# Kernel optimization log

Hardware: AMD Instinct MI355X
Metric: run time of the kernel (lower is better)

Reference implementation:

```python
import jax, jax.numpy as jnp
import numpy as np

N_NODES = 50000
N_EDGES = 800000
IN_DIM = 128
HID = 32
HEADS = 4
OUT_DIM = 64
NEG_SLOPE = 0.2
EPS = 1e-16


def _gat_conv(x, src, dst, W, a_src, a_dst, b, heads, ch):
    """PyG GATConv (with self-loops already appended to src/dst), concat=True."""
    N = x.shape[0]
    h = (x @ W).reshape(N, heads, ch)                      # [N,H,C]
    alpha_s = jnp.einsum('nhc,hc->nh', h, a_src)           # [N,H]
    alpha_d = jnp.einsum('nhc,hc->nh', h, a_dst)           # [N,H]
    e = jax.nn.leaky_relu(alpha_s[src] + alpha_d[dst], NEG_SLOPE)  # [E,H]
    emax = jax.ops.segment_max(e, dst, num_segments=N)     # segment softmax over dst
    ex = jnp.exp(e - emax[dst])
    denom = jax.ops.segment_sum(ex, dst, num_segments=N)
    alpha = ex / (denom[dst] + EPS)                        # [E,H]
    out = jax.ops.segment_sum(h[src] * alpha[:, :, None], dst, num_segments=N)
    return out.reshape(N, heads * ch) + b


def setup_inputs() -> dict:
    key = jax.random.key(0)
    ks = jax.random.split(key, 16)
    x = jax.random.normal(ks[0], (N_NODES, IN_DIM), dtype=jnp.float32)
    edge_index = jax.random.randint(ks[1], (2, N_EDGES), 0, N_NODES, dtype=jnp.int64)

    def glorot(k, shape):
        fan = sum(shape[-2:]) if len(shape) > 1 else shape[-1]
        return jax.random.normal(k, shape, dtype=jnp.float32) * np.sqrt(2.0 / fan)

    # layer 0: IN_DIM -> HID x HEADS
    W0 = glorot(ks[2], (IN_DIM, HEADS * HID))
    as0 = glorot(ks[3], (HEADS, HID))
    ad0 = glorot(ks[4], (HEADS, HID))
    b0 = jnp.zeros((HEADS * HID,), jnp.float32)
    # layer 1: HID*HEADS -> HID x HEADS
    W1 = glorot(ks[5], (HEADS * HID, HEADS * HID))
    as1 = glorot(ks[6], (HEADS, HID))
    ad1 = glorot(ks[7], (HEADS, HID))
    b1 = jnp.zeros((HEADS * HID,), jnp.float32)
    # layer 2: HID*HEADS -> OUT_DIM, heads=1
    W2 = glorot(ks[8], (HEADS * HID, OUT_DIM))
    as2 = glorot(ks[9], (1, OUT_DIM))
    ad2 = glorot(ks[10], (1, OUT_DIM))
    b2 = jnp.zeros((OUT_DIM,), jnp.float32)
    return {"x": x, "edge_index": edge_index,
            "W0": W0, "as0": as0, "ad0": ad0, "b0": b0,
            "W1": W1, "as1": as1, "ad1": ad1, "b1": b1,
            "W2": W2, "as2": as2, "ad2": ad2, "b2": b2}


def reference(x, edge_index, W0, as0, ad0, b0, W1, as1, ad1, b1, W2, as2, ad2, b2):
    N = x.shape[0]
    # PyG GATConv default add_self_loops=True
    loops = jnp.arange(N, dtype=edge_index.dtype)
    src = jnp.concatenate([edge_index[0], loops])
    dst = jnp.concatenate([edge_index[1], loops])
    h = _gat_conv(x, src, dst, W0, as0, ad0, b0, HEADS, HID)
    h = _gat_conv(h, src, dst, W1, as1, ad1, b1, HEADS, HID)
    h = _gat_conv(h, src, dst, W2, as2, ad2, b2, 1, OUT_DIM)
    return h
```

## Files before the change

kernel.cpp:

```cpp
#include <hip/hip_runtime.h>
#include <hip/hip_fp16.h>
#include <cstdint>
#include <cstddef>

#define NEG_SLOPE 0.2f
#define EPS_F 1e-16f

static __device__ __forceinline__ float leaky(float x) { return x > 0.f ? x : NEG_SLOPE * x; }


__global__ __launch_bounds__(1024) void scan_k(const int* __restrict__ cnt, int* __restrict__ off, int N) {
    __shared__ int wsum[16];
    int tid = threadIdx.x;
    int lane = tid & 63, wid = tid >> 6;
    int running = 0;
    for (int base = 0; base < N; base += 1024) {
        int i = base + tid;
        int v = (i < N) ? cnt[i] : 0;
        int iv = v;
        #pragma unroll
        for (int d = 1; d < 64; d <<= 1) {
            int t = __shfl_up(iv, d);
            if (lane >= d) iv += t;
        }
        if (lane == 63) wsum[wid] = iv;
        __syncthreads();
        if (tid < 16) {
            int s = wsum[tid];
            #pragma unroll
            for (int d = 1; d < 16; d <<= 1) {
                int t = __shfl_up(s, d);
                if (tid >= d) s += t;
            }
            wsum[tid] = s;
        }
        __syncthreads();
        int add = wid ? wsum[wid - 1] : 0;
        if (i < N) off[i + 1] = running + add + iv;
        int ct = wsum[15];
        __syncthreads();
        running += ct;
    }
    if (tid == 0) off[0] = 0;
}


__global__ __launch_bounds__(256) void partB_k(const int* __restrict__ src, const int* __restrict__ dst,
                                               const int* __restrict__ starts, int* __restrict__ packed,
                                               int E, int nbuk) {
    __shared__ int lcnt[256];
    __shared__ int lbase[256];
    const int blk = blockIdx.x;
    for (int i = threadIdx.x; i < nbuk; i += 256) { lcnt[i] = 0; lbase[i] = starts[i * 256 + blk]; }
    __syncthreads();
    const int chunk = (E + 255) / 256;
    const int base = blk * chunk, end = min(base + chunk, E);
    for (int i = base + (int)threadIdx.x; i < end; i += 256) {
        int d = dst[i], s = src[i];
        int b = d >> 8;
        int slot = atomicAdd(&lcnt[b], 1);
        packed[lbase[b] + slot] = s | ((d & 255) << 16);
    }
}


__global__ __launch_bounds__(256) void partC_k(const int* __restrict__ packed, const int* __restrict__ starts,
                                               int* __restrict__ off, int* __restrict__ esrc,
                                               int N, int E, int nbuk) {
    __shared__ int lcnt[256];
    __shared__ int lpre[256];
    const int b = blockIdx.x;
    const int bstart = starts[b * 256];
    const int bend = (b + 1 < nbuk) ? starts[(b + 1) * 256] : E;
    const int tid = threadIdx.x;
    lcnt[tid] = 0;
    __syncthreads();
    for (int i = bstart + tid; i < bend; i += 256) atomicAdd(&lcnt[packed[i] >> 16], 1);
    __syncthreads();
    if (tid < 64) {
        int v0 = lcnt[tid * 4], v1 = lcnt[tid * 4 + 1], v2 = lcnt[tid * 4 + 2], v3 = lcnt[tid * 4 + 3];
        int s = v0 + v1 + v2 + v3;
        int inc = s;
        #pragma unroll
        for (int d = 1; d < 64; d <<= 1) {
            int t = __shfl_up(inc, d);
            if (tid >= d) inc += t;
        }
        int ex = inc - s;
        lpre[tid * 4] = ex;
        lpre[tid * 4 + 1] = ex + v0;
        lpre[tid * 4 + 2] = ex + v0 + v1;
        lpre[tid * 4 + 3] = ex + v0 + v1 + v2;
    }
    __syncthreads();
    const int n0 = b << 8;
    const int nn = min(256, N - n0);
    if (tid < nn) off[n0 + tid] = bstart + lpre[tid];
    if (b == 0 && tid == 0) off[N] = E;
    lcnt[tid] = 0;
    __syncthreads();
    for (int i = bstart + tid; i < bend; i += 256) {
        int p = packed[i];
        int ld = p >> 16;
        int slot = atomicAdd(&lcnt[ld], 1);
        esrc[bstart + lpre[ld] + slot] = p & 0xFFFF;
    }
}


template <int M, int H>
__device__ __forceinline__ void gemm_body(float* xsT, float* wt,
                                          const float* __restrict__ X, const float* __restrict__ W,
                                          const float* __restrict__ a_s, const float* __restrict__ a_d,
                                          __half* __restrict__ O, float* __restrict__ aS,
                                          float* __restrict__ aD, int N, int bid) {
    constexpr int K = 128, BK = 16, ROWS = 128;
    constexpr int CPT = 8;
    constexpr int CT = M / CPT;
    constexpr int RPT = ROWS / (256 / CT);
    constexpr int XP = ROWS + 4;
    constexpr int C = M / H;
    constexpr int REDW = C / CPT;

    const int tid = threadIdx.x;
    const int cc = tid % CT;
    const int rr = tid / CT;
    const int row0 = bid * ROWS;

    float acc[RPT][CPT];
    #pragma unroll
    for (int r = 0; r < RPT; ++r)
        #pragma unroll
        for (int j = 0; j < CPT; ++j) acc[r][j] = 0.f;

    for (int k0 = 0; k0 < K; k0 += BK) {
        #pragma unroll
        for (int t = tid; t < ROWS * (BK / 4); t += 256) {
            int r = t >> 2;
            int kk = t & 3;
            int row = row0 + r;
            float4 v = make_float4(0.f, 0.f, 0.f, 0.f);
            if (row < N) v = *reinterpret_cast<const float4*>(&X[(size_t)row * K + k0 + kk * 4]);
            xsT[(kk * 4 + 0) * XP + r] = v.x;
            xsT[(kk * 4 + 1) * XP + r] = v.y;
            xsT[(kk * 4 + 2) * XP + r] = v.z;
            xsT[(kk * 4 + 3) * XP + r] = v.w;
        }
        #pragma unroll
        for (int t = tid; t < BK * (M / 4); t += 256) {
            int c4 = t % (M / 4);
            int k = t / (M / 4);
            *reinterpret_cast<float4*>(&wt[k * M + c4 * 4]) =
                *reinterpret_cast<const float4*>(&W[(size_t)(k0 + k) * M + c4 * 4]);
        }
        __syncthreads();
        #pragma unroll
        for (int k = 0; k < BK; ++k) {
            float xr[RPT];
            #pragma unroll
            for (int r4 = 0; r4 < RPT; r4 += 4) {
                float4 xv = *reinterpret_cast<const float4*>(&xsT[k * XP + rr * RPT + r4]);
                xr[r4 + 0] = xv.x; xr[r4 + 1] = xv.y; xr[r4 + 2] = xv.z; xr[r4 + 3] = xv.w;
            }
            float wv[CPT];
            #pragma unroll
            for (int c4 = 0; c4 < CPT; c4 += 4) {
                float4 w4 = *reinterpret_cast<const float4*>(&wt[k * M + cc * CPT + c4]);
                wv[c4 + 0] = w4.x; wv[c4 + 1] = w4.y; wv[c4 + 2] = w4.z; wv[c4 + 3] = w4.w;
            }
            #pragma unroll
            for (int r = 0; r < RPT; ++r)
                #pragma unroll
                for (int j = 0; j < CPT; ++j)
                    acc[r][j] = fmaf(xr[r], wv[j], acc[r][j]);
        }
        __syncthreads();
    }

    float asr[CPT], adr[CPT];
    #pragma unroll
    for (int c4 = 0; c4 < CPT; c4 += 4) {
        float4 t1 = *reinterpret_cast<const float4*>(a_s + cc * CPT + c4);
        asr[c4 + 0] = t1.x; asr[c4 + 1] = t1.y; asr[c4 + 2] = t1.z; asr[c4 + 3] = t1.w;
        float4 t2 = *reinterpret_cast<const float4*>(a_d + cc * CPT + c4);
        adr[c4 + 0] = t2.x; adr[c4 + 1] = t2.y; adr[c4 + 2] = t2.z; adr[c4 + 3] = t2.w;
    }
    const int head = (cc * CPT) / C;

    #pragma unroll
    for (int r = 0; r < RPT; ++r) {
        int row = row0 + rr * RPT + r;
        float ps = 0.f, pd = 0.f;
        #pragma unroll
        for (int j = 0; j < CPT; ++j) {
            ps = fmaf(acc[r][j], asr[j], ps);
            pd = fmaf(acc[r][j], adr[j], pd);
        }
        #pragma unroll
        for (int d = 1; d < REDW; d <<= 1) {
            ps += __shfl_xor(ps, d);
            pd += __shfl_xor(pd, d);
        }
        if (row < N) {
            __half2 p0 = __float22half2_rn(make_float2(acc[r][0], acc[r][1]));
            __half2 p1 = __float22half2_rn(make_float2(acc[r][2], acc[r][3]));
            __half2 p2 = __float22half2_rn(make_float2(acc[r][4], acc[r][5]));
            __half2 p3 = __float22half2_rn(make_float2(acc[r][6], acc[r][7]));
            uint4 pk;
            pk.x = *reinterpret_cast<unsigned*>(&p0);
            pk.y = *reinterpret_cast<unsigned*>(&p1);
            pk.z = *reinterpret_cast<unsigned*>(&p2);
            pk.w = *reinterpret_cast<unsigned*>(&p3);
            *reinterpret_cast<uint4*>(&O[(size_t)row * M + cc * CPT]) = pk;
            if ((cc & (REDW - 1)) == 0) {
                aS[(size_t)row * H + head] = ps;
                aD[(size_t)row * H + head] = pd;
            }
        }
    }
}

template <int M, int H>
__global__ __launch_bounds__(256, 2) void gemm_k(const float* __restrict__ X, const float* __restrict__ W,
                                                 const float* __restrict__ a_s, const float* __restrict__ a_d,
                                                 __half* __restrict__ O, float* __restrict__ aS,
                                                 float* __restrict__ aD, int N) {
    __shared__ float smem[16 * 132 + 16 * M];
    gemm_body<M, H>(smem, smem + 16 * 132, X, W, a_s, a_d, O, aS, aD, N, blockIdx.x);
}

template <int M, int H>
__global__ __launch_bounds__(256, 2) void gemm_hist_k(const float* __restrict__ X, const float* __restrict__ W,
                                                      const float* __restrict__ a_s, const float* __restrict__ a_d,
                                                      __half* __restrict__ O, float* __restrict__ aS,
                                                      float* __restrict__ aD, int N,
                                                      const int* __restrict__ dst, int E,
                                                      int* __restrict__ cnts, int gemmGrid, int nbuk) {
    __shared__ float smem[16 * 132 + 16 * M];
    if ((int)blockIdx.x < gemmGrid) {
        gemm_body<M, H>(smem, smem + 16 * 132, X, W, a_s, a_d, O, aS, aD, N, blockIdx.x);
    } else {
        int* lcnt = (int*)smem;
        const int blk = blockIdx.x - gemmGrid;
        for (int i = threadIdx.x; i < nbuk; i += 256) lcnt[i] = 0;
        __syncthreads();
        const int chunk = (E + 255) / 256;
        const int base = blk * chunk, end = min(base + chunk, E);
        for (int i = base + (int)threadIdx.x; i < end; i += 256) atomicAdd(&lcnt[dst[i] >> 8], 1);
        __syncthreads();
        for (int b = threadIdx.x; b < nbuk; b += 256) cnts[b * 256 + blk] = lcnt[b];
    }
}


template <int H, int C>
__global__ __launch_bounds__(256) void agg_k(const __half* __restrict__ h, const float* __restrict__ aS,
                                             const float* __restrict__ aD, const int* __restrict__ off,
                                             const int* __restrict__ esrc, const float* __restrict__ bias,
                                             float* __restrict__ out, int N) {
    constexpr int M = H * C;
    constexpr int CPL = M / 32;
    __shared__ float wlds[4][2][32][H];
    __shared__ int   slds[4][2][32];
    const int wslot = threadIdx.x >> 6;
    const int lane  = threadIdx.x & 63;
    const int g     = lane >> 5;
    const int lg    = lane & 31;
    const int node  = (blockIdx.x * 4 + wslot) * 2 + g;
    const bool valid = node < N;
    const int nd = valid ? node : N - 1;

    float adv[H], asv[H];
    if constexpr (H == 4) {
        float4 t = *reinterpret_cast<const float4*>(aD + (size_t)nd * 4);
        adv[0] = t.x; adv[1] = t.y; adv[2] = t.z; adv[3] = t.w;
        float4 u = *reinterpret_cast<const float4*>(aS + (size_t)nd * 4);
        asv[0] = u.x; asv[1] = u.y; asv[2] = u.z; asv[3] = u.w;
    } else {
        adv[0] = aD[nd]; asv[0] = aS[nd];
    }
    float eself[H];
    #pragma unroll
    for (int q = 0; q < H; ++q) eself[q] = leaky(asv[q] + adv[q]);

    const int s0 = off[nd], s1 = off[nd + 1];
    const int deg = s1 - s0;

    if (__all(deg < 32)) {
        const int sv = (lg < deg) ? esrc[s0 + lg] : nd;
        if constexpr (H == 4) {
            float4 u = *reinterpret_cast<const float4*>(aS + (size_t)sv * 4);
            float4 wv;
            if (lg < deg) {
                wv.x = __expf(leaky(u.x + adv[0]));
                wv.y = __expf(leaky(u.y + adv[1]));
                wv.z = __expf(leaky(u.z + adv[2]));
                wv.w = __expf(leaky(u.w + adv[3]));
            } else if (lg == deg) {
                wv = make_float4(__expf(eself[0]), __expf(eself[1]), __expf(eself[2]), __expf(eself[3]));
            } else {
                wv = make_float4(0.f, 0.f, 0.f, 0.f);
            }
            *reinterpret_cast<float4*>(&wlds[wslot][g][lg][0]) = wv;
        } else {
            float u = aS[sv];
            wlds[wslot][g][lg][0] = (lg < deg) ? __expf(leaky(u + adv[0]))
                                  : (lg == deg) ? __expf(eself[0]) : 0.f;
        }
        slds[wslot][g][lg] = sv;
        asm volatile("s_waitcnt lgkmcnt(0)" ::: "memory");

        const int cnt = deg + 1;
        const int cmax = max(cnt, __shfl_xor(cnt, 32));
        const int ch0 = lg * CPL;
        const int hd = ch0 / C;
        float wsum = 0.f;

        if constexpr (CPL == 4) {
            float acc0 = 0.f, acc1 = 0.f, acc2 = 0.f, acc3 = 0.f;
            uint2 A[8], B[8];
            auto issue = [&](uint2 (&buf)[8], int j) {
                #pragma unroll
                for (int t = 0; t < 8; ++t) {
                    int s = slds[wslot][g][j + t];
                    buf[t] = *reinterpret_cast<const uint2*>(h + (size_t)s * M + ch0);
                }
            };
            auto consume = [&](uint2 (&buf)[8], int j) {
                #pragma unroll
                for (int t = 0; t < 8; ++t) {
                    float wq = wlds[wslot][g][j + t][hd];
                    wsum += wq;
                    float2 fa = __half22float2(*reinterpret_cast<__half2*>(&buf[t].x));
                    float2 fb = __half22float2(*reinterpret_cast<__half2*>(&buf[t].y));
                    acc0 = fmaf(wq, fa.x, acc0);
                    acc1 = fmaf(wq, fa.y, acc1);
                    acc2 = fmaf(wq, fb.x, acc2);
                    acc3 = fmaf(wq, fb.y, acc3);
                }
            };
            issue(A, 0);
            if (cmax > 8) issue(B, 8);
            consume(A, 0);
            if (cmax > 8) {
                if (cmax > 16) issue(A, 16);
                consume(B, 8);
                if (cmax > 16) {
                    if (cmax > 24) issue(B, 24);
                    consume(A, 16);
                    if (cmax > 24) consume(B, 24);
                }
            }
            if (valid) {
                float inv = 1.f / (wsum + EPS_F);
                float4 bb = *reinterpret_cast<const float4*>(bias + ch0);
                *reinterpret_cast<float4*>(out + (size_t)nd * M + ch0) =
                    make_float4(acc0 * inv + bb.x, acc1 * inv + bb.y, acc2 * inv + bb.z, acc3 * inv + bb.w);
            }
        } else {
            float acc0 = 0.f, acc1 = 0.f;
            unsigned A[8], B[8];
            auto issue = [&](unsigned (&buf)[8], int j) {
                #pragma unroll
                for (int t = 0; t < 8; ++t) {
                    int s = slds[wslot][g][j + t];
                    buf[t] = *reinterpret_cast<const unsigned*>(h + (size_t)s * M + ch0);
                }
            };
            auto consume = [&](unsigned (&buf)[8], int j) {
                #pragma unroll
                for (int t = 0; t < 8; ++t) {
                    float wq = wlds[wslot][g][j + t][0];
                    wsum += wq;
                    float2 fa = __half22float2(*reinterpret_cast<__half2*>(&buf[t]));
                    acc0 = fmaf(wq, fa.x, acc0);
                    acc1 = fmaf(wq, fa.y, acc1);
                }
            };
            issue(A, 0);
            if (cmax > 8) issue(B, 8);
            consume(A, 0);
            if (cmax > 8) {
                if (cmax > 16) issue(A, 16);
                consume(B, 8);
                if (cmax > 16) {
                    if (cmax > 24) issue(B, 24);
                    consume(A, 16);
                    if (cmax > 24) consume(B, 24);
                }
            }
            if (valid) {
                float inv = 1.f / (wsum + EPS_F);
                float2 bb = *reinterpret_cast<const float2*>(bias + ch0);
                *reinterpret_cast<float2*>(out + (size_t)nd * M + ch0) =
                    make_float2(acc0 * inv + bb.x, acc1 * inv + bb.y);
            }
        }
    } else {
        constexpr int CPL64 = M / 64;
        const int ch = lane * CPL64;
        const int hh = ch / C;
        #pragma unroll 1
        for (int i = 0; i < 2; ++i) {
            int fn = (blockIdx.x * 4 + wslot) * 2 + i;
            if (fn >= N) continue;
            float fadv[H], fes[H];
            if constexpr (H == 4) {
                float4 t = *reinterpret_cast<const float4*>(aD + (size_t)fn * 4);
                fadv[0] = t.x; fadv[1] = t.y; fadv[2] = t.z; fadv[3] = t.w;
                float4 u = *reinterpret_cast<const float4*>(aS + (size_t)fn * 4);
                fes[0] = leaky(u.x + t.x); fes[1] = leaky(u.y + t.y);
                fes[2] = leaky(u.z + t.z); fes[3] = leaky(u.w + t.w);
            } else {
                fadv[0] = aD[fn];
                fes[0] = leaky(aS[fn] + fadv[0]);
            }
            int fs0 = off[fn], fs1 = off[fn + 1];
            float m[H], ds[H];
            #pragma unroll
            for (int q = 0; q < H; ++q) { m[q] = fes[q]; ds[q] = 0.f; }
            for (int e = fs0 + lane; e < fs1; e += 64) {
                int s = esrc[e];
                if constexpr (H == 4) {
                    float4 u = *reinterpret_cast<const float4*>(aS + (size_t)s * 4);
                    float evv[4] = {u.x, u.y, u.z, u.w};
                    #pragma unroll
                    for (int q = 0; q < 4; ++q) {
                        float ee = leaky(evv[q] + fadv[q]);
                        float nm = fmaxf(m[q], ee);
                        ds[q] = ds[q] * __expf(m[q] - nm) + __expf(ee - nm);
                        m[q] = nm;
                    }
                } else {
                    float ee = leaky(aS[s] + fadv[0]);
                    float nm = fmaxf(m[0], ee);
                    ds[0] = ds[0] * __expf(m[0] - nm) + __expf(ee - nm);
                    m[0] = nm;
                }
            }
            #pragma unroll
            for (int q = 0; q < H; ++q) {
                #pragma unroll
                for (int d = 1; d < 64; d <<= 1) {
                    float om = __shfl_xor(m[q], d);
                    float od = __shfl_xor(ds[q], d);
                    float nm = fmaxf(m[q], om);
                    ds[q] = ds[q] * __expf(m[q] - nm) + od * __expf(om - nm);
                    m[q] = nm;
                }
                ds[q] += __expf(fes[q] - m[q]);
            }
            float a0 = 0.f, a1 = 0.f;
            for (int e = fs0; e < fs1; ++e) {
                int s = esrc[e];
                float wq = __expf(leaky(aS[(size_t)s * H + hh] + fadv[hh]) - m[hh]);
                if constexpr (CPL64 == 2) {
                    float2 f = __half22float2(*reinterpret_cast<const __half2*>(h + (size_t)s * M + ch));
                    a0 = fmaf(wq, f.x, a0);
                    a1 = fmaf(wq, f.y, a1);
                } else {
                    a0 = fmaf(wq, __half2float(h[(size_t)s * M + ch]), a0);
                }
            }
            {
                float wq = __expf(fes[hh] - m[hh]);
                if constexpr (CPL64 == 2) {
                    float2 f = __half22float2(*reinterpret_cast<const __half2*>(h + (size_t)fn * M + ch));
                    a0 = fmaf(wq, f.x, a0);
                    a1 = fmaf(wq, f.y, a1);
                } else {
                    a0 = fmaf(wq, __half2float(h[(size_t)fn * M + ch]), a0);
                }
            }
            float inv = 1.f / (ds[hh] + EPS_F);
            if constexpr (CPL64 == 2) {
                *reinterpret_cast<float2*>(out + (size_t)fn * M + ch) =
                    make_float2(a0 * inv + bias[ch], a1 * inv + bias[ch + 1]);
            } else {
                out[(size_t)fn * M + ch] = a0 * inv + bias[ch];
            }
        }
    }
}


extern "C" void kernel_launch(void* const* d_in, const int* in_sizes, int n_in,
                              void* d_out, int out_size, void* d_ws, size_t ws_size,
                              hipStream_t stream) {
    const float* x   = (const float*)d_in[0];
    const int*   ei  = (const int*)d_in[1];
    const float* W0  = (const float*)d_in[2];
    const float* as0 = (const float*)d_in[3];
    const float* ad0 = (const float*)d_in[4];
    const float* b0  = (const float*)d_in[5];
    const float* W1  = (const float*)d_in[6];
    const float* as1 = (const float*)d_in[7];
    const float* ad1 = (const float*)d_in[8];
    const float* b1  = (const float*)d_in[9];
    const float* W2  = (const float*)d_in[10];
    const float* as2 = (const float*)d_in[11];
    const float* ad2 = (const float*)d_in[12];
    const float* b2  = (const float*)d_in[13];

    const int N = in_sizes[0] / 128;
    const int E = in_sizes[1] / 2;
    const int* esrc_in = ei;
    const int* edst_in = ei + E;
    const int NBUK = (N + 255) >> 8;
    const int NBLKB = 256;

    char* w = (char*)d_ws;
    auto carve = [&](size_t bytes) -> char* {
        char* p = w;
        w += (bytes + 255) & ~(size_t)255;
        return p;
    };
    int*    off    = (int*)carve((size_t)(N + 1) * 4);
    int*    es     = (int*)carve((size_t)E * 4);
    int*    cnts   = (int*)carve((size_t)NBUK * NBLKB * 4);
    int*    starts = (int*)carve(((size_t)NBUK * NBLKB + 1) * 4);
    int*    packed = (int*)carve((size_t)E * 4);
    float*  aS     = (float*)carve((size_t)N * 4 * sizeof(float));
    float*  aD     = (float*)carve((size_t)N * 4 * sizeof(float));
    __half* bufH   = (__half*)carve((size_t)N * 128 * sizeof(__half));
    float*  bufO   = (float*)carve((size_t)N * 128 * sizeof(float));
    (void)ws_size; (void)n_in; (void)out_size;

    const int GEMM_GRID = (N + 127) / 128;
    const int AGG_GRID = (N + 7) / 8;

    gemm_hist_k<128, 4><<<GEMM_GRID + NBLKB, 256, 0, stream>>>(x, W0, as0, ad0, bufH, aS, aD, N,
                                                               edst_in, E, cnts, GEMM_GRID, NBUK);
    scan_k<<<1, 1024, 0, stream>>>(cnts, starts, NBUK * NBLKB);
    partB_k<<<NBLKB, 256, 0, stream>>>(esrc_in, edst_in, starts, packed, E, NBUK);
    partC_k<<<NBUK, 256, 0, stream>>>(packed, starts, off, es, N, E, NBUK);

    agg_k<4, 32><<<AGG_GRID, 256, 0, stream>>>(bufH, aS, aD, off, es, b0, bufO, N);

    gemm_k<128, 4><<<GEMM_GRID, 256, 0, stream>>>(bufO, W1, as1, ad1, bufH, aS, aD, N);
    agg_k<4, 32><<<AGG_GRID, 256, 0, stream>>>(bufH, aS, aD, off, es, b1, bufO, N);

    gemm_k<64, 1><<<GEMM_GRID, 256, 0, stream>>>(bufO, W2, as2, ad2, bufH, aS, aD, N);
    agg_k<1, 64><<<AGG_GRID, 256, 0, stream>>>(bufH, aS, aD, off, es, b2, (float*)d_out, N);
}
```

Measured before the change: 273.9 us.

## Store intermediate layer outputs in fp16 and hoist first gather before weight computation

Intermediate aggregation outputs (bufO) become fp16 instead of fp32. The following GEMMs read half inputs and convert them to float when staging into shared memory, which halves the write and read traffic between layers. In the low-degree aggregation path, the first batch of neighbor feature gathers is issued before the attention weights are computed and stored to LDS, so memory latency overlaps with the exp math. The cost is extra rounding of hidden activations to fp16.

```diff
diff --git a/kernel.cpp b/kernel.cpp
--- a/kernel.cpp
+++ b/kernel.cpp
@@ -62,7 +62,6 @@
         packed[lbase[b] + slot] = s | ((d & 255) << 16);
     }
 }
-
 
 __global__ __launch_bounds__(256) void partC_k(const int* __restrict__ packed, const int* __restrict__ starts,
                                                int* __restrict__ off, int* __restrict__ esrc,
@@ -108,9 +107,9 @@
 }
 
 
-template <int M, int H>
+template <int M, int H, typename XT>
 __device__ __forceinline__ void gemm_body(float* xsT, float* wt,
-                                          const float* __restrict__ X, const float* __restrict__ W,
+                                          const XT* __restrict__ X, const float* __restrict__ W,
                                           const float* __restrict__ a_s, const float* __restrict__ a_d,
                                           __half* __restrict__ O, float* __restrict__ aS,
                                           float* __restrict__ aD, int N, int bid) {
@@ -140,7 +139,16 @@
             int kk = t & 3;
             int row = row0 + r;
             float4 v = make_float4(0.f, 0.f, 0.f, 0.f);
-            if (row < N) v = *reinterpret_cast<const float4*>(&X[(size_t)row * K + k0 + kk * 4]);
+            if (row < N) {
+                if constexpr (sizeof(XT) == 2) {
+                    uint2 raw = *reinterpret_cast<const uint2*>(&X[(size_t)row * K + k0 + kk * 4]);
+                    float2 fa = __half22float2(*reinterpret_cast<__half2*>(&raw.x));
+                    float2 fb = __half22float2(*reinterpret_cast<__half2*>(&raw.y));
+                    v = make_float4(fa.x, fa.y, fb.x, fb.y);
+                } else {
+                    v = *reinterpret_cast<const float4*>(&X[(size_t)row * K + k0 + kk * 4]);
+                }
+            }
             xsT[(kk * 4 + 0) * XP + r] = v.x;
             xsT[(kk * 4 + 1) * XP + r] = v.y;
             xsT[(kk * 4 + 2) * XP + r] = v.z;
@@ -220,13 +228,13 @@
     }
 }
 
-template <int M, int H>
-__global__ __launch_bounds__(256, 2) void gemm_k(const float* __restrict__ X, const float* __restrict__ W,
+template <int M, int H, typename XT>
+__global__ __launch_bounds__(256, 2) void gemm_k(const XT* __restrict__ X, const float* __restrict__ W,
                                                  const float* __restrict__ a_s, const float* __restrict__ a_d,
                                                  __half* __restrict__ O, float* __restrict__ aS,
                                                  float* __restrict__ aD, int N) {
     __shared__ float smem[16 * 132 + 16 * M];
-    gemm_body<M, H>(smem, smem + 16 * 132, X, W, a_s, a_d, O, aS, aD, N, blockIdx.x);
+    gemm_body<M, H, XT>(smem, smem + 16 * 132, X, W, a_s, a_d, O, aS, aD, N, blockIdx.x);
 }
 
 template <int M, int H>
@@ -238,7 +246,7 @@
                                                       int* __restrict__ cnts, int gemmGrid, int nbuk) {
     __shared__ float smem[16 * 132 + 16 * M];
     if ((int)blockIdx.x < gemmGrid) {
-        gemm_body<M, H>(smem, smem + 16 * 132, X, W, a_s, a_d, O, aS, aD, N, blockIdx.x);
+        gemm_body<M, H, float>(smem, smem + 16 * 132, X, W, a_s, a_d, O, aS, aD, N, blockIdx.x);
     } else {
         int* lcnt = (int*)smem;
         const int blk = blockIdx.x - gemmGrid;
@@ -253,11 +261,11 @@
 }
 
 
-template <int H, int C>
+template <int H, int C, typename OutT>
 __global__ __launch_bounds__(256) void agg_k(const __half* __restrict__ h, const float* __restrict__ aS,
                                              const float* __restrict__ aD, const int* __restrict__ off,
                                              const int* __restrict__ esrc, const float* __restrict__ bias,
-                                             float* __restrict__ out, int N) {
+                                             OutT* __restrict__ out, int N) {
     constexpr int M = H * C;
     constexpr int CPL = M / 32;
     __shared__ float wlds[4][2][32][H];
@@ -288,37 +296,38 @@
 
     if (__all(deg < 32)) {
         const int sv = (lg < deg) ? esrc[s0 + lg] : nd;
-        if constexpr (H == 4) {
-            float4 u = *reinterpret_cast<const float4*>(aS + (size_t)sv * 4);
-            float4 wv;
-            if (lg < deg) {
-                wv.x = __expf(leaky(u.x + adv[0]));
-                wv.y = __expf(leaky(u.y + adv[1]));
-                wv.z = __expf(leaky(u.z + adv[2]));
-                wv.w = __expf(leaky(u.w + adv[3]));
-            } else if (lg == deg) {
-                wv = make_float4(__expf(eself[0]), __expf(eself[1]), __expf(eself[2]), __expf(eself[3]));
-            } else {
-                wv = make_float4(0.f, 0.f, 0.f, 0.f);
-            }
-            *reinterpret_cast<float4*>(&wlds[wslot][g][lg][0]) = wv;
-        } else {
-            float u = aS[sv];
-            wlds[wslot][g][lg][0] = (lg < deg) ? __expf(leaky(u + adv[0]))
-                                  : (lg == deg) ? __expf(eself[0]) : 0.f;
-        }
-        slds[wslot][g][lg] = sv;
-        asm volatile("s_waitcnt lgkmcnt(0)" ::: "memory");
-
+        const int ch0 = lg * CPL;
+        const int hd = ch0 / C;
         const int cnt = deg + 1;
         const int cmax = max(cnt, __shfl_xor(cnt, 32));
-        const int ch0 = lg * CPL;
-        const int hd = ch0 / C;
         float wsum = 0.f;
 
         if constexpr (CPL == 4) {
+            uint2 A[8], B[8];
+            #pragma unroll
+            for (int t = 0; t < 8; ++t) {
+                int s = __shfl(sv, t, 32);
+                A[t] = *reinterpret_cast<const uint2*>(h + (size_t)s * M + ch0);
+            }
+            {
+                float4 u = *reinterpret_cast<const float4*>(aS + (size_t)sv * 4);
+                float4 wv;
+                if (lg < deg) {
+                    wv.x = __expf(leaky(u.x + adv[0]));
+                    wv.y = __expf(leaky(u.y + adv[1]));
+                    wv.z = __expf(leaky(u.z + adv[2]));
+                    wv.w = __expf(leaky(u.w + adv[3]));
+                } else if (lg == deg) {
+                    wv = make_float4(__expf(eself[0]), __expf(eself[1]), __expf(eself[2]), __expf(eself[3]));
+                } else {
+                    wv = make_float4(0.f, 0.f, 0.f, 0.f);
+                }
+                *reinterpret_cast<float4*>(&wlds[wslot][g][lg][0]) = wv;
+                slds[wslot][g][lg] = sv;
+            }
+            asm volatile("s_waitcnt lgkmcnt(0)" ::: "memory");
+
             float acc0 = 0.f, acc1 = 0.f, acc2 = 0.f, acc3 = 0.f;
-            uint2 A[8], B[8];
             auto issue = [&](uint2 (&buf)[8], int j) {
                 #pragma unroll
                 for (int t = 0; t < 8; ++t) {
@@ -339,7 +348,6 @@
                     acc3 = fmaf(wq, fb.y, acc3);
                 }
             };
-            issue(A, 0);
             if (cmax > 8) issue(B, 8);
             consume(A, 0);
             if (cmax > 8) {
@@ -354,12 +362,35 @@
             if (valid) {
                 float inv = 1.f / (wsum + EPS_F);
                 float4 bb = *reinterpret_cast<const float4*>(bias + ch0);
-                *reinterpret_cast<float4*>(out + (size_t)nd * M + ch0) =
-                    make_float4(acc0 * inv + bb.x, acc1 * inv + bb.y, acc2 * inv + bb.z, acc3 * inv + bb.w);
+                float o0 = acc0 * inv + bb.x, o1 = acc1 * inv + bb.y;
+                float o2 = acc2 * inv + bb.z, o3 = acc3 * inv + bb.w;
+                if constexpr (sizeof(OutT) == 4) {
+                    *reinterpret_cast<float4*>((float*)out + (size_t)nd * M + ch0) = make_float4(o0, o1, o2, o3);
+                } else {
+                    __half2 q0 = __float22half2_rn(make_float2(o0, o1));
+                    __half2 q1 = __float22half2_rn(make_float2(o2, o3));
+                    uint2 pk;
+                    pk.x = *reinterpret_cast<unsigned*>(&q0);
+                    pk.y = *reinterpret_cast<unsigned*>(&q1);
+                    *reinterpret_cast<uint2*>((__half*)out + (size_t)nd * M + ch0) = pk;
+                }
             }
         } else {
+            unsigned A[8], B[8];
+            #pragma unroll
+            for (int t = 0; t < 8; ++t) {
+                int s = __shfl(sv, t, 32);
+                A[t] = *reinterpret_cast<const unsigned*>(h + (size_t)s * M + ch0);
+            }
+            {
+                float u = aS[sv];
+                wlds[wslot][g][lg][0] = (lg < deg) ? __expf(leaky(u + adv[0]))
+                                      : (lg == deg) ? __expf(eself[0]) : 0.f;
+                slds[wslot][g][lg] = sv;
+            }
+            asm volatile("s_waitcnt lgkmcnt(0)" ::: "memory");
+
             float acc0 = 0.f, acc1 = 0.f;
-            unsigned A[8], B[8];
             auto issue = [&](unsigned (&buf)[8], int j) {
                 #pragma unroll
                 for (int t = 0; t < 8; ++t) {
@@ -377,7 +408,6 @@
                     acc1 = fmaf(wq, fa.y, acc1);
                 }
             };
-            issue(A, 0);
             if (cmax > 8) issue(B, 8);
             consume(A, 0);
             if (cmax > 8) {
@@ -391,9 +421,15 @@
             }
             if (valid) {
                 float inv = 1.f / (wsum + EPS_F);
-                float2 bb = *reinterpret_cast<const float2*>(bias + ch0);
-                *reinterpret_cast<float2*>(out + (size_t)nd * M + ch0) =
-                    make_float2(acc0 * inv + bb.x, acc1 * inv + bb.y);
+                float o0 = acc0 * inv + bias[ch0];
+                float o1 = acc1 * inv + bias[ch0 + 1];
+                if constexpr (sizeof(OutT) == 4) {
+                    *reinterpret_cast<float2*>((float*)out + (size_t)nd * M + ch0) = make_float2(o0, o1);
+                } else {
+                    __half2 q0 = __float22half2_rn(make_float2(o0, o1));
+                    *reinterpret_cast<unsigned*>((__half*)out + (size_t)nd * M + ch0) =
+                        *reinterpret_cast<unsigned*>(&q0);
+                }
             }
         }
     } else {
@@ -474,10 +510,18 @@
             }
             float inv = 1.f / (ds[hh] + EPS_F);
             if constexpr (CPL64 == 2) {
-                *reinterpret_cast<float2*>(out + (size_t)fn * M + ch) =
-                    make_float2(a0 * inv + bias[ch], a1 * inv + bias[ch + 1]);
+                float o0 = a0 * inv + bias[ch], o1 = a1 * inv + bias[ch + 1];
+                if constexpr (sizeof(OutT) == 4) {
+                    *reinterpret_cast<float2*>((float*)out + (size_t)fn * M + ch) = make_float2(o0, o1);
+                } else {
+                    __half2 q0 = __float22half2_rn(make_float2(o0, o1));
+                    *reinterpret_cast<unsigned*>((__half*)out + (size_t)fn * M + ch) =
+                        *reinterpret_cast<unsigned*>(&q0);
+                }
             } else {
-                out[(size_t)fn * M + ch] = a0 * inv + bias[ch];
+                float o0 = a0 * inv + bias[ch];
+                if constexpr (sizeof(OutT) == 4) ((float*)out)[(size_t)fn * M + ch] = o0;
+                else ((__half*)out)[(size_t)fn * M + ch] = __float2half_rn(o0);
             }
         }
     }
@@ -523,7 +567,7 @@
     float*  aS     = (float*)carve((size_t)N * 4 * sizeof(float));
     float*  aD     = (float*)carve((size_t)N * 4 * sizeof(float));
     __half* bufH   = (__half*)carve((size_t)N * 128 * sizeof(__half));
-    float*  bufO   = (float*)carve((size_t)N * 128 * sizeof(float));
+    __half* bufO   = (__half*)carve((size_t)N * 128 * sizeof(__half));
     (void)ws_size; (void)n_in; (void)out_size;
 
     const int GEMM_GRID = (N + 127) / 128;
@@ -535,11 +579,11 @@
     partB_k<<<NBLKB, 256, 0, stream>>>(esrc_in, edst_in, starts, packed, E, NBUK);
     partC_k<<<NBUK, 256, 0, stream>>>(packed, starts, off, es, N, E, NBUK);
 
-    agg_k<4, 32><<<AGG_GRID, 256, 0, stream>>>(bufH, aS, aD, off, es, b0, bufO, N);
-
-    gemm_k<128, 4><<<GEMM_GRID, 256, 0, stream>>>(bufO, W1, as1, ad1, bufH, aS, aD, N);
-    agg_k<4, 32><<<AGG_GRID, 256, 0, stream>>>(bufH, aS, aD, off, es, b1, bufO, N);
-
-    gemm_k<64, 1><<<GEMM_GRID, 256, 0, stream>>>(bufO, W2, as2, ad2, bufH, aS, aD, N);
-    agg_k<1, 64><<<AGG_GRID, 256, 0, stream>>>(bufH, aS, aD, off, es, b2, (float*)d_out, N);
-}
+    agg_k<4, 32, __half><<<AGG_GRID, 256, 0, stream>>>(bufH, aS, aD, off, es, b0, bufO, N);
+
+    gemm_k<128, 4, __half><<<GEMM_GRID, 256, 0, stream>>>(bufO, W1, as1, ad1, bufH, aS, aD, N);
+    agg_k<4, 32, __half><<<AGG_GRID, 256, 0, stream>>>(bufH, aS, aD, off, es, b1, bufO, N);
+
+    gemm_k<64, 1, __half><<<GEMM_GRID, 256, 0, stream>>>(bufO, W2, as2, ad2, bufH, aS, aD, N);
+    agg_k<1, 64, float><<<AGG_GRID, 256, 0, stream>>>(bufH, aS, aD, off, es, b2, (float*)d_out, N);
+}
```

Measured after the change: 271.5 us. Within noise of the previous version (-0.9%).

## Split aggregation into per-channel-slice passes, store intermediates in fp16, shrink partition blocks

Applied to the files above, without the earlier changes.

The aggregation kernel is restructured so each block handles one 32-channel slice (pass) of a node group. Each lane owns one channel and fetches its neighbour source ids with shuffles instead of staging them in LDS. Blocks are interleaved so the passes for the same nodes run close together, which should improve gather locality in L2 and cut per-thread register pressure. The intermediate activations between layers are stored in fp16, and the GEMM gains an fp16 input path, halving that traffic at some cost in precision. The edge-partition block count drops from 256 to 64. The trade-off is that attention scores are recomputed per pass, and the high-degree fallback path is now per-lane and serial.

```diff
diff --git a/kernel.cpp b/kernel.cpp
--- a/kernel.cpp
+++ b/kernel.cpp
@@ -5,6 +5,7 @@
 
 #define NEG_SLOPE 0.2f
 #define EPS_F 1e-16f
+#define NBLKB 64
 
 static __device__ __forceinline__ float leaky(float x) { return x > 0.f ? x : NEG_SLOPE * x; }
 
@@ -51,9 +52,9 @@
     __shared__ int lcnt[256];
     __shared__ int lbase[256];
     const int blk = blockIdx.x;
-    for (int i = threadIdx.x; i < nbuk; i += 256) { lcnt[i] = 0; lbase[i] = starts[i * 256 + blk]; }
+    for (int i = threadIdx.x; i < nbuk; i += 256) { lcnt[i] = 0; lbase[i] = starts[i * NBLKB + blk]; }
     __syncthreads();
-    const int chunk = (E + 255) / 256;
+    const int chunk = (E + NBLKB - 1) / NBLKB;
     const int base = blk * chunk, end = min(base + chunk, E);
     for (int i = base + (int)threadIdx.x; i < end; i += 256) {
         int d = dst[i], s = src[i];
@@ -63,15 +64,14 @@
     }
 }
 
-
 __global__ __launch_bounds__(256) void partC_k(const int* __restrict__ packed, const int* __restrict__ starts,
                                                int* __restrict__ off, int* __restrict__ esrc,
                                                int N, int E, int nbuk) {
     __shared__ int lcnt[256];
     __shared__ int lpre[256];
     const int b = blockIdx.x;
-    const int bstart = starts[b * 256];
-    const int bend = (b + 1 < nbuk) ? starts[(b + 1) * 256] : E;
+    const int bstart = starts[b * NBLKB];
+    const int bend = (b + 1 < nbuk) ? starts[(b + 1) * NBLKB] : E;
     const int tid = threadIdx.x;
     lcnt[tid] = 0;
     __syncthreads();
@@ -108,9 +108,9 @@
 }
 
 
-template <int M, int H>
+template <int M, int H, typename XT>
 __device__ __forceinline__ void gemm_body(float* xsT, float* wt,
-                                          const float* __restrict__ X, const float* __restrict__ W,
+                                          const XT* __restrict__ X, const float* __restrict__ W,
                                           const float* __restrict__ a_s, const float* __restrict__ a_d,
                                           __half* __restrict__ O, float* __restrict__ aS,
                                           float* __restrict__ aD, int N, int bid) {
@@ -140,7 +140,16 @@
             int kk = t & 3;
             int row = row0 + r;
             float4 v = make_float4(0.f, 0.f, 0.f, 0.f);
-            if (row < N) v = *reinterpret_cast<const float4*>(&X[(size_t)row * K + k0 + kk * 4]);
+            if (row < N) {
+                if constexpr (sizeof(XT) == 2) {
+                    uint2 raw = *reinterpret_cast<const uint2*>(&X[(size_t)row * K + k0 + kk * 4]);
+                    float2 fa = __half22float2(*reinterpret_cast<__half2*>(&raw.x));
+                    float2 fb = __half22float2(*reinterpret_cast<__half2*>(&raw.y));
+                    v = make_float4(fa.x, fa.y, fb.x, fb.y);
+                } else {
+                    v = *reinterpret_cast<const float4*>(&X[(size_t)row * K + k0 + kk * 4]);
+                }
+            }
             xsT[(kk * 4 + 0) * XP + r] = v.x;
             xsT[(kk * 4 + 1) * XP + r] = v.y;
             xsT[(kk * 4 + 2) * XP + r] = v.z;
@@ -220,13 +229,13 @@
     }
 }
 
-template <int M, int H>
-__global__ __launch_bounds__(256, 2) void gemm_k(const float* __restrict__ X, const float* __restrict__ W,
+template <int M, int H, typename XT>
+__global__ __launch_bounds__(256, 2) void gemm_k(const XT* __restrict__ X, const float* __restrict__ W,
                                                  const float* __restrict__ a_s, const float* __restrict__ a_d,
                                                  __half* __restrict__ O, float* __restrict__ aS,
                                                  float* __restrict__ aD, int N) {
     __shared__ float smem[16 * 132 + 16 * M];
-    gemm_body<M, H>(smem, smem + 16 * 132, X, W, a_s, a_d, O, aS, aD, N, blockIdx.x);
+    gemm_body<M, H, XT>(smem, smem + 16 * 132, X, W, a_s, a_d, O, aS, aD, N, blockIdx.x);
 }
 
 template <int M, int H>
@@ -238,246 +247,152 @@
                                                       int* __restrict__ cnts, int gemmGrid, int nbuk) {
     __shared__ float smem[16 * 132 + 16 * M];
     if ((int)blockIdx.x < gemmGrid) {
-        gemm_body<M, H>(smem, smem + 16 * 132, X, W, a_s, a_d, O, aS, aD, N, blockIdx.x);
+        gemm_body<M, H, float>(smem, smem + 16 * 132, X, W, a_s, a_d, O, aS, aD, N, blockIdx.x);
     } else {
         int* lcnt = (int*)smem;
         const int blk = blockIdx.x - gemmGrid;
         for (int i = threadIdx.x; i < nbuk; i += 256) lcnt[i] = 0;
         __syncthreads();
-        const int chunk = (E + 255) / 256;
+        const int chunk = (E + NBLKB - 1) / NBLKB;
         const int base = blk * chunk, end = min(base + chunk, E);
         for (int i = base + (int)threadIdx.x; i < end; i += 256) atomicAdd(&lcnt[dst[i] >> 8], 1);
         __syncthreads();
-        for (int b = threadIdx.x; b < nbuk; b += 256) cnts[b * 256 + blk] = lcnt[b];
-    }
-}
-
-
-template <int H, int C>
+        for (int b = threadIdx.x; b < nbuk; b += 256) cnts[b * NBLKB + blk] = lcnt[b];
+    }
+}
+
+
+template <int H, int C, int NPASS, typename OutT>
 __global__ __launch_bounds__(256) void agg_k(const __half* __restrict__ h, const float* __restrict__ aS,
                                              const float* __restrict__ aD, const int* __restrict__ off,
                                              const int* __restrict__ esrc, const float* __restrict__ bias,
-                                             float* __restrict__ out, int N) {
+                                             OutT* __restrict__ out, int N, int nodeBlocks) {
     constexpr int M = H * C;
-    constexpr int CPL = M / 32;
-    __shared__ float wlds[4][2][32][H];
-    __shared__ int   slds[4][2][32];
+    constexpr int PCH = M / NPASS;
+    constexpr int SUBS = 8 / NPASS;
+    static_assert(PCH == 32, "one channel per lane");
+    __shared__ float wlds[4][2][32];
+
+    const int G = blockIdx.x & 7;
+    const int pass = G % NPASS;
+    const int sub = G / NPASS;
+    const int nb = ((int)blockIdx.x >> 3) * SUBS + sub;
+    if (nb >= nodeBlocks) return;
+
     const int wslot = threadIdx.x >> 6;
-    const int lane  = threadIdx.x & 63;
-    const int g     = lane >> 5;
-    const int lg    = lane & 31;
-    const int node  = (blockIdx.x * 4 + wslot) * 2 + g;
+    const int lane = threadIdx.x & 63;
+    const int g = lane >> 5, lg = lane & 31;
+    const int node = (nb * 4 + wslot) * 2 + g;
     const bool valid = node < N;
     const int nd = valid ? node : N - 1;
 
-    float adv[H], asv[H];
-    if constexpr (H == 4) {
-        float4 t = *reinterpret_cast<const float4*>(aD + (size_t)nd * 4);
-        adv[0] = t.x; adv[1] = t.y; adv[2] = t.z; adv[3] = t.w;
-        float4 u = *reinterpret_cast<const float4*>(aS + (size_t)nd * 4);
-        asv[0] = u.x; asv[1] = u.y; asv[2] = u.z; asv[3] = u.w;
-    } else {
-        adv[0] = aD[nd]; asv[0] = aS[nd];
-    }
-    float eself[H];
-    #pragma unroll
-    for (int q = 0; q < H; ++q) eself[q] = leaky(asv[q] + adv[q]);
+    const int ch = pass * PCH + lg;
+    const int hd = ch / C;
+    const float advh = aD[(size_t)nd * H + hd];
+    const float asvh = aS[(size_t)nd * H + hd];
+    const float es = leaky(asvh + advh);
 
     const int s0 = off[nd], s1 = off[nd + 1];
     const int deg = s1 - s0;
 
     if (__all(deg < 32)) {
         const int sv = (lg < deg) ? esrc[s0 + lg] : nd;
-        if constexpr (H == 4) {
-            float4 u = *reinterpret_cast<const float4*>(aS + (size_t)sv * 4);
-            float4 wv;
-            if (lg < deg) {
-                wv.x = __expf(leaky(u.x + adv[0]));
-                wv.y = __expf(leaky(u.y + adv[1]));
-                wv.z = __expf(leaky(u.z + adv[2]));
-                wv.w = __expf(leaky(u.w + adv[3]));
-            } else if (lg == deg) {
-                wv = make_float4(__expf(eself[0]), __expf(eself[1]), __expf(eself[2]), __expf(eself[3]));
-            } else {
-                wv = make_float4(0.f, 0.f, 0.f, 0.f);
-            }
-            *reinterpret_cast<float4*>(&wlds[wslot][g][lg][0]) = wv;
-        } else {
-            float u = aS[sv];
-            wlds[wslot][g][lg][0] = (lg < deg) ? __expf(leaky(u + adv[0]))
-                                  : (lg == deg) ? __expf(eself[0]) : 0.f;
-        }
-        slds[wslot][g][lg] = sv;
-        asm volatile("s_waitcnt lgkmcnt(0)" ::: "memory");
-
         const int cnt = deg + 1;
         const int cmax = max(cnt, __shfl_xor(cnt, 32));
-        const int ch0 = lg * CPL;
-        const int hd = ch0 / C;
-        float wsum = 0.f;
-
-        if constexpr (CPL == 4) {
-            float acc0 = 0.f, acc1 = 0.f, acc2 = 0.f, acc3 = 0.f;
-            uint2 A[8], B[8];
-            auto issue = [&](uint2 (&buf)[8], int j) {
+
+        __half A[8], B[8], Cb[8];
+        #pragma unroll
+        for (int t = 0; t < 8; ++t) {
+            int s = __shfl(sv, t, 32);
+            A[t] = h[(size_t)s * M + ch];
+        }
+        if (cmax > 8) {
+            #pragma unroll
+            for (int t = 0; t < 8; ++t) {
+                int s = __shfl(sv, 8 + t, 32);
+                B[t] = h[(size_t)s * M + ch];
+            }
+        }
+        if (cmax > 16) {
+            #pragma unroll
+            for (int t = 0; t < 8; ++t) {
+                int s = __shfl(sv, 16 + t, 32);
+                Cb[t] = h[(size_t)s * M + ch];
+            }
+        }
+        {
+            float u = aS[(size_t)sv * H + hd];
+            float w = (lg < deg) ? __expf(leaky(u + advh))
+                    : (lg == deg) ? __expf(es) : 0.f;
+            wlds[wslot][g][lg] = w;
+        }
+        asm volatile("s_waitcnt lgkmcnt(0)" ::: "memory");
+
+        float acc = 0.f, wsum = 0.f;
+        auto consume = [&](__half (&buf)[8], int j) {
+            #pragma unroll
+            for (int t = 0; t < 8; ++t) {
+                float wq = wlds[wslot][g][j + t];
+                wsum += wq;
+                acc = fmaf(wq, __half2float(buf[t]), acc);
+            }
+        };
+        consume(A, 0);
+        if (cmax > 8) {
+            if (cmax > 24) {
                 #pragma unroll
                 for (int t = 0; t < 8; ++t) {
-                    int s = slds[wslot][g][j + t];
-                    buf[t] = *reinterpret_cast<const uint2*>(h + (size_t)s * M + ch0);
+                    int s = __shfl(sv, 24 + t, 32);
+                    A[t] = h[(size_t)s * M + ch];
                 }
-            };
-            auto consume = [&](uint2 (&buf)[8], int j) {
-                #pragma unroll
-                for (int t = 0; t < 8; ++t) {
-                    float wq = wlds[wslot][g][j + t][hd];
-                    wsum += wq;
-                    float2 fa = __half22float2(*reinterpret_cast<__half2*>(&buf[t].x));
-                    float2 fb = __half22float2(*reinterpret_cast<__half2*>(&buf[t].y));
-                    acc0 = fmaf(wq, fa.x, acc0);
-                    acc1 = fmaf(wq, fa.y, acc1);
-                    acc2 = fmaf(wq, fb.x, acc2);
-                    acc3 = fmaf(wq, fb.y, acc3);
-                }
-            };
-            issue(A, 0);
-            if (cmax > 8) issue(B, 8);
-            consume(A, 0);
-            if (cmax > 8) {
-                if (cmax > 16) issue(A, 16);
-                consume(B, 8);
-                if (cmax > 16) {
-                    if (cmax > 24) issue(B, 24);
-                    consume(A, 16);
-                    if (cmax > 24) consume(B, 24);
-                }
-            }
-            if (valid) {
-                float inv = 1.f / (wsum + EPS_F);
-                float4 bb = *reinterpret_cast<const float4*>(bias + ch0);
-                *reinterpret_cast<float4*>(out + (size_t)nd * M + ch0) =
-                    make_float4(acc0 * inv + bb.x, acc1 * inv + bb.y, acc2 * inv + bb.z, acc3 * inv + bb.w);
-            }
-        } else {
-            float acc0 = 0.f, acc1 = 0.f;
-            unsigned A[8], B[8];
-            auto issue = [&](unsigned (&buf)[8], int j) {
-                #pragma unroll
-                for (int t = 0; t < 8; ++t) {
-                    int s = slds[wslot][g][j + t];
-                    buf[t] = *reinterpret_cast<const unsigned*>(h + (size_t)s * M + ch0);
-                }
-            };
-            auto consume = [&](unsigned (&buf)[8], int j) {
-                #pragma unroll
-                for (int t = 0; t < 8; ++t) {
-                    float wq = wlds[wslot][g][j + t][0];
-                    wsum += wq;
-                    float2 fa = __half22float2(*reinterpret_cast<__half2*>(&buf[t]));
-                    acc0 = fmaf(wq, fa.x, acc0);
-                    acc1 = fmaf(wq, fa.y, acc1);
-                }
-            };
-            issue(A, 0);
-            if (cmax > 8) issue(B, 8);
-            consume(A, 0);
-            if (cmax > 8) {
-                if (cmax > 16) issue(A, 16);
-                consume(B, 8);
-                if (cmax > 16) {
-                    if (cmax > 24) issue(B, 24);
-                    consume(A, 16);
-                    if (cmax > 24) consume(B, 24);
-                }
-            }
-            if (valid) {
-                float inv = 1.f / (wsum + EPS_F);
-                float2 bb = *reinterpret_cast<const float2*>(bias + ch0);
-                *reinterpret_cast<float2*>(out + (size_t)nd * M + ch0) =
-                    make_float2(acc0 * inv + bb.x, acc1 * inv + bb.y);
+            }
+            consume(B, 8);
+            if (cmax > 16) {
+                consume(Cb, 16);
+                if (cmax > 24) consume(A, 24);
+            }
+        }
+        if (valid) {
+            float o = acc / (wsum + EPS_F) + bias[ch];
+            if constexpr (sizeof(OutT) == 2) {
+                __half hv = __float2half_rn(o);
+                __builtin_nontemporal_store(*reinterpret_cast<unsigned short*>(&hv),
+                                            reinterpret_cast<unsigned short*>((__half*)out + (size_t)nd * M + ch));
+            } else {
+                __builtin_nontemporal_store(o, (float*)out + (size_t)nd * M + ch);
             }
         }
     } else {
-        constexpr int CPL64 = M / 64;
-        const int ch = lane * CPL64;
-        const int hh = ch / C;
-        #pragma unroll 1
-        for (int i = 0; i < 2; ++i) {
-            int fn = (blockIdx.x * 4 + wslot) * 2 + i;
-            if (fn >= N) continue;
-            float fadv[H], fes[H];
-            if constexpr (H == 4) {
-                float4 t = *reinterpret_cast<const float4*>(aD + (size_t)fn * 4);
-                fadv[0] = t.x; fadv[1] = t.y; fadv[2] = t.z; fadv[3] = t.w;
-                float4 u = *reinterpret_cast<const float4*>(aS + (size_t)fn * 4);
-                fes[0] = leaky(u.x + t.x); fes[1] = leaky(u.y + t.y);
-                fes[2] = leaky(u.z + t.z); fes[3] = leaky(u.w + t.w);
+        if (valid) {
+            float m = es, dsum = 0.f;
+            for (int e = s0 + lg; e < s1; e += 32) {
+                float uu = aS[(size_t)esrc[e] * H + hd];
+                float ee = leaky(uu + advh);
+                float nm = fmaxf(m, ee);
+                dsum = dsum * __expf(m - nm) + __expf(ee - nm);
+                m = nm;
+            }
+            #pragma unroll
+            for (int d = 1; d < 32; d <<= 1) {
+                float om = __shfl_xor(m, d, 32);
+                float od = __shfl_xor(dsum, d, 32);
+                float nm = fmaxf(m, om);
+                dsum = dsum * __expf(m - nm) + od * __expf(om - nm);
+                m = nm;
+            }
+            dsum += __expf(es - m);
+            float acc = 0.f;
+            for (int e = s0; e < s1; ++e) {
+                int s = esrc[e];
+                float wq = __expf(leaky(aS[(size_t)s * H + hd] + advh) - m);
+                acc = fmaf(wq, __half2float(h[(size_t)s * M + ch]), acc);
+            }
+            acc = fmaf(__expf(es - m), __half2float(h[(size_t)nd * M + ch]), acc);
+            float o = acc / (dsum + EPS_F) + bias[ch];
+            if constexpr (sizeof(OutT) == 2) {
+                ((__half*)out)[(size_t)nd * M + ch] = __float2half_rn(o);
             } else {
-                fadv[0] = aD[fn];
-                fes[0] = leaky(aS[fn] + fadv[0]);
-            }
-            int fs0 = off[fn], fs1 = off[fn + 1];
-            float m[H], ds[H];
-            #pragma unroll
-            for (int q = 0; q < H; ++q) { m[q] = fes[q]; ds[q] = 0.f; }
-            for (int e = fs0 + lane; e < fs1; e += 64) {
-                int s = esrc[e];
-                if constexpr (H == 4) {
-                    float4 u = *reinterpret_cast<const float4*>(aS + (size_t)s * 4);
-                    float evv[4] = {u.x, u.y, u.z, u.w};
-                    #pragma unroll
-                    for (int q = 0; q < 4; ++q) {
-                        float ee = leaky(evv[q] + fadv[q]);
-                        float nm = fmaxf(m[q], ee);
-                        ds[q] = ds[q] * __expf(m[q] - nm) + __expf(ee - nm);
-                        m[q] = nm;
-                    }
-                } else {
-                    float ee = leaky(aS[s] + fadv[0]);
-                    float nm = fmaxf(m[0], ee);
-                    ds[0] = ds[0] * __expf(m[0] - nm) + __expf(ee - nm);
-                    m[0] = nm;
-                }
-            }
-            #pragma unroll
-            for (int q = 0; q < H; ++q) {
-                #pragma unroll
-                for (int d = 1; d < 64; d <<= 1) {
-                    float om = __shfl_xor(m[q], d);
-                    float od = __shfl_xor(ds[q], d);
-                    float nm = fmaxf(m[q], om);
-                    ds[q] = ds[q] * __expf(m[q] - nm) + od * __expf(om - nm);
-                    m[q] = nm;
-                }
-                ds[q] += __expf(fes[q] - m[q]);
-            }
-            float a0 = 0.f, a1 = 0.f;
-            for (int e = fs0; e < fs1; ++e) {
-                int s = esrc[e];
-                float wq = __expf(leaky(aS[(size_t)s * H + hh] + fadv[hh]) - m[hh]);
-                if constexpr (CPL64 == 2) {
-                    float2 f = __half22float2(*reinterpret_cast<const __half2*>(h + (size_t)s * M + ch));
-                    a0 = fmaf(wq, f.x, a0);
-                    a1 = fmaf(wq, f.y, a1);
-                } else {
-                    a0 = fmaf(wq, __half2float(h[(size_t)s * M + ch]), a0);
-                }
-            }
-            {
-                float wq = __expf(fes[hh] - m[hh]);
-                if constexpr (CPL64 == 2) {
-                    float2 f = __half22float2(*reinterpret_cast<const __half2*>(h + (size_t)fn * M + ch));
-                    a0 = fmaf(wq, f.x, a0);
-                    a1 = fmaf(wq, f.y, a1);
-                } else {
-                    a0 = fmaf(wq, __half2float(h[(size_t)fn * M + ch]), a0);
-                }
-            }
-            float inv = 1.f / (ds[hh] + EPS_F);
-            if constexpr (CPL64 == 2) {
-                *reinterpret_cast<float2*>(out + (size_t)fn * M + ch) =
-                    make_float2(a0 * inv + bias[ch], a1 * inv + bias[ch + 1]);
-            } else {
-                out[(size_t)fn * M + ch] = a0 * inv + bias[ch];
+                ((float*)out)[(size_t)nd * M + ch] = o;
             }
         }
     }
@@ -507,7 +422,6 @@
     const int* esrc_in = ei;
     const int* edst_in = ei + E;
     const int NBUK = (N + 255) >> 8;
-    const int NBLKB = 256;
 
     char* w = (char*)d_ws;
     auto carve = [&](size_t bytes) -> char* {
@@ -523,11 +437,13 @@
     float*  aS     = (float*)carve((size_t)N * 4 * sizeof(float));
     float*  aD     = (float*)carve((size_t)N * 4 * sizeof(float));
     __half* bufH   = (__half*)carve((size_t)N * 128 * sizeof(__half));
-    float*  bufO   = (float*)carve((size_t)N * 128 * sizeof(float));
+    __half* bufO   = (__half*)carve((size_t)N * 128 * sizeof(__half));
     (void)ws_size; (void)n_in; (void)out_size;
 
     const int GEMM_GRID = (N + 127) / 128;
-    const int AGG_GRID = (N + 7) / 8;
+    const int NB = (N + 7) / 8;
+    const int GRID4 = ((NB + 1) / 2) * 8;
+    const int GRID2 = ((NB + 3) / 4) * 8;
 
     gemm_hist_k<128, 4><<<GEMM_GRID + NBLKB, 256, 0, stream>>>(x, W0, as0, ad0, bufH, aS, aD, N,
                                                                edst_in, E, cnts, GEMM_GRID, NBUK);
@@ -535,11 +451,11 @@
     partB_k<<<NBLKB, 256, 0, stream>>>(esrc_in, edst_in, starts, packed, E, NBUK);
     partC_k<<<NBUK, 256, 0, stream>>>(packed, starts, off, es, N, E, NBUK);
 
-    agg_k<4, 32><<<AGG_GRID, 256, 0, stream>>>(bufH, aS, aD, off, es, b0, bufO, N);
-
-    gemm_k<128, 4><<<GEMM_GRID, 256, 0, stream>>>(bufO, W1, as1, ad1, bufH, aS, aD, N);
-    agg_k<4, 32><<<AGG_GRID, 256, 0, stream>>>(bufH, aS, aD, off, es, b1, bufO, N);
-
-    gemm_k<64, 1><<<GEMM_GRID, 256, 0, stream>>>(bufO, W2, as2, ad2, bufH, aS, aD, N);
-    agg_k<1, 64><<<AGG_GRID, 256, 0, stream>>>(bufH, aS, aD, off, es, b2, (float*)d_out, N);
-}
+    agg_k<4, 32, 4, __half><<<GRID4, 256, 0, stream>>>(bufH, aS, aD, off, es, b0, bufO, N, NB);
+
+    gemm_k<128, 4, __half><<<GEMM_GRID, 256, 0, stream>>>(bufO, W1, as1, ad1, bufH, aS, aD, N);
+    agg_k<4, 32, 4, __half><<<GRID4, 256, 0, stream>>>(bufH, aS, aD, off, es, b1, bufO, N, NB);
+
+    gemm_k<64, 1, __half><<<GEMM_GRID, 256, 0, stream>>>(bufO, W2, as2, ad2, bufH, aS, aD, N);
+    agg_k<1, 64, 2, float><<<GRID2, 256, 0, stream>>>(bufH, aS, aD, off, es, b2, (float*)d_out, N, NB);
+}
```

After: 283.5 us. 1.03x slower.
